# Performance work log

Hardware: AMD Instinct MI355X
Metric: run time of the kernel (lower is better)

Reference implementation:

```python
import jax, jax.numpy as jnp
import numpy as np

IMG = 224   # img_size
K = 8       # num_bands
E = 256     # embed_dim


def _radial_masks(size, k):
    # Faithful to torch _create_radial_masks: center = size//2, max_r = size/sqrt(2)
    center = size // 2
    y, x = jnp.meshgrid(jnp.arange(size), jnp.arange(size), indexing='ij')
    r = jnp.sqrt(((x - center) ** 2 + (y - center) ** 2).astype(jnp.float32))
    max_r = size / np.sqrt(2.0)
    step = np.float32(max_r / k)
    i = jnp.arange(k, dtype=jnp.float32)[:, None, None]
    masks = ((r[None] >= step * i) & (r[None] < step * (i + 1.0))).astype(jnp.float32)
    return masks  # [K, H, W]


def setup_inputs() -> dict:
    key = jax.random.key(0)
    ks = jax.random.split(key, 3)
    x = jax.random.normal(ks[0], (64, 3, IMG, IMG), dtype=jnp.float32)
    W1 = jax.random.normal(ks[1], (3, E), dtype=jnp.float32) * 0.3
    b1 = jnp.zeros((E,), jnp.float32)
    gamma = jnp.ones((E,), jnp.float32)
    beta = jnp.zeros((E,), jnp.float32)
    W2 = jax.random.normal(ks[2], (E, E), dtype=jnp.float32) * (1.0 / np.sqrt(E))
    b2 = jnp.zeros((E,), jnp.float32)
    return {"x": x, "W1": W1, "b1": b1, "gamma": gamma, "beta": beta, "W2": W2, "b2": b2}


def reference(x, W1, b1, gamma, beta, W2, b2):
    masks = _radial_masks(IMG, K)                    # [K,H,W], binary, non-overlapping
    x_gray = x.mean(axis=1)                          # [B,H,W]
    fft = jnp.fft.fftshift(jnp.fft.fft2(x_gray), axes=(-2, -1))
    mag = jnp.log1p(jnp.abs(fft))                    # log(1+|F|)
    mu = mag.mean(axis=(1, 2), keepdims=True)
    sd = jnp.std(mag, axis=(1, 2), keepdims=True, ddof=1) + 1e-6  # torch .std is unbiased
    magn = (mag - mu) / sd                           # [B,H,W]

    msum = masks.sum(axis=(1, 2))                    # [K], true mask pixel counts
    mask_sums = msum + 1e-6
    s1 = jnp.einsum('bhw,khw->bk', magn, masks)      # per-band sum
    s2 = jnp.einsum('bhw,khw->bk', magn * magn, masks)
    means = s1 / mask_sums
    # sum((magn - means)^2 * mask) = s2 - 2*means*s1 + means^2 * msum  (exact expansion)
    var_num = s2 - 2.0 * means * s1 + (means ** 2) * msum
    stds = jnp.sqrt(var_num / mask_sums + 1e-6)
    # masked_fill(mask==0, -1e9) then amax over H,W
    maxs = jnp.max(jnp.where(masks[None] > 0, magn[:, None], -1e9), axis=(2, 3))

    feats = jnp.stack([means, stds, maxs], axis=-1)  # [B,K,3]
    h = feats @ W1 + b1                              # [B,K,E]
    hm = h.mean(axis=-1, keepdims=True)
    hv = h.var(axis=-1, keepdims=True)
    h = (h - hm) / jnp.sqrt(hv + 1e-5) * gamma + beta  # LayerNorm, eps=1e-5
    h = jax.nn.relu(h)
    return h @ W2 + b2                               # [B,K,E]
```

## Files before the change

### kernel.cpp

```cpp
#include <hip/hip_runtime.h>
#include <math.h>

#define IMG 224
#define NPIX 50176
#define BATCH 64
#define EDIM 256

typedef _Float16 f16;
typedef __attribute__((ext_vector_type(8))) _Float16 f16x8;
typedef __attribute__((ext_vector_type(4))) _Float16 f16x4;
typedef __attribute__((ext_vector_type(4))) float f32x4;
typedef unsigned int u32;


#define GLD16(gp, lp)                                                          \
  __builtin_amdgcn_global_load_lds(                                            \
      (const __attribute__((address_space(1))) u32*)(gp),                      \
      (__attribute__((address_space(3))) u32*)(lp), 16, 0, 0)

__global__ __launch_bounds__(256) void gemmA_kernel(const float* __restrict__ x,
                                                    const f16* __restrict__ B1,
                                                    f16* __restrict__ B2t) {
  __shared__ f16 As[2][64][64];
  __shared__ f16 Bs[2][256][64];
  int m0 = blockIdx.x * 64;
  int tid = threadIdx.x;
  int lane = tid & 63, wid = tid >> 6;
  int wr = wid >> 1, wc = wid & 1;

  int arow = tid >> 2;
  int aseg = tid & 3;
  int am = m0 + arow;
  int ab = am / 224, ah = am - ab * 224;
  const float* px = x + (size_t)ab * 3 * NPIX + ah * IMG;
  int s0 = (aseg * 2) ^ (arow & 7);
  int s1 = (aseg * 2 + 1) ^ (arow & 7);

  int srow = lane >> 3;
  int sk8 = (lane & 7) ^ srow;

  f32x4 xl[3][4];

  f32x4 acc[2][8];
#pragma unroll
  for (int i = 0; i < 2; ++i)
#pragma unroll
    for (int j = 0; j < 8; ++j) acc[i][j] = (f32x4){0.f, 0.f, 0.f, 0.f};

  auto issueA = [&](int t) {
    int kb = t * 64 + aseg * 16;
    if (kb < 224) {
#pragma unroll
      for (int c = 0; c < 3; ++c)
#pragma unroll
        for (int q = 0; q < 4; ++q)
          xl[c][q] = *(const f32x4*)(px + c * NPIX + kb + q * 4);
    }
  };
  auto issueB = [&](int bufi, int t) {
    int k0 = t * 64;
#pragma unroll
    for (int ci = 0; ci < 8; ++ci) {
      int j = wid * 8 + ci;
      GLD16(B1 + (size_t)(j * 8 + srow) * 256 + k0 + sk8 * 8,
            &Bs[bufi][0][0] + j * 512);
    }
  };
  auto writeA = [&](int bufi, int t) {
    int kb = t * 64 + aseg * 16;
    f16x8 h0, h1;
    if (kb < 224) {
#pragma unroll
      for (int j = 0; j < 8; ++j) {
        int q = j >> 2, r = j & 3;
        h0[j] = (f16)((xl[0][q][r] + xl[1][q][r] + xl[2][q][r]) * (1.0f / 3.0f));
      }
#pragma unroll
      for (int j = 0; j < 8; ++j) {
        int q = 2 + (j >> 2), r = j & 3;
        h1[j] = (f16)((xl[0][q][r] + xl[1][q][r] + xl[2][q][r]) * (1.0f / 3.0f));
      }
    } else {
#pragma unroll
      for (int j = 0; j < 8; ++j) { h0[j] = (f16)0.f; h1[j] = (f16)0.f; }
    }
    *(f16x8*)&As[bufi][arow][s0 * 8] = h0;
    *(f16x8*)&As[bufi][arow][s1 * 8] = h1;
  };

  issueA(0);
  issueB(0, 0);
#pragma unroll 1
  for (int t = 0; t < 4; ++t) {
    int cur = t & 1;
    asm volatile("s_waitcnt vmcnt(0)" ::: "memory");
    writeA(cur, t);
    asm volatile("s_waitcnt lgkmcnt(0)" ::: "memory");
    __builtin_amdgcn_s_barrier();
    if (t < 3) { issueA(t + 1); issueB(cur ^ 1, t + 1); }
#pragma unroll
    for (int kk = 0; kk < 2; ++kk) {
      f16x8 af[2], bfr[8];
#pragma unroll
      for (int mi = 0; mi < 2; ++mi) {
        int row = wr * 32 + mi * 16 + (lane & 15);
        int slot = (kk * 4 + (lane >> 4)) ^ (row & 7);
        af[mi] = *(const f16x8*)&As[cur][row][slot * 8];
      }
#pragma unroll
      for (int nj = 0; nj < 8; ++nj) {
        int row = wc * 128 + nj * 16 + (lane & 15);
        int slot = (kk * 4 + (lane >> 4)) ^ (row & 7);
        bfr[nj] = *(const f16x8*)&Bs[cur][row][slot * 8];
      }
#pragma unroll
      for (int mi = 0; mi < 2; ++mi)
#pragma unroll
        for (int nj = 0; nj < 8; ++nj)
          acc[mi][nj] = __builtin_amdgcn_mfma_f32_16x16x32_f16(
              af[mi], bfr[nj], acc[mi][nj], 0, 0, 0);
    }
    __builtin_amdgcn_s_barrier();
  }

  int mbase = m0 + wr * 32, nbase = wc * 128;
#pragma unroll
  for (int mi = 0; mi < 2; ++mi) {
#pragma unroll
    for (int nj = 0; nj < 8; ++nj) {
      int c = nbase + nj * 16 + (lane & 15);
      if (c >= 226) continue;
      int m = mbase + mi * 16 + ((lane >> 4) << 2);
      int b = m / 224;
      int h = m - b * 224;
      int v = c, kb = h;
      if (c >= 113) { v = c - 113; kb = 224 + h; }
      size_t off = (size_t)(b * 128 + v) * 448 + kb;
      f32x4 y = acc[mi][nj];
      f16x4 hv;
#pragma unroll
      for (int r = 0; r < 4; ++r) hv[r] = (f16)y[r];
      *(f16x4*)&B2t[off] = hv;
    }
  }
}

template <int LDK, int NT>
__device__ __forceinline__ void gemm_core(const f16* __restrict__ A,
                                          const f16* __restrict__ B,
                                          int m0, int n0,
                                          f16 (*As)[64][64], f16 (*Bs)[128][64],
                                          f32x4 acc[2][4]) {
  int tid = threadIdx.x;
  int lane = tid & 63, wid = tid >> 6;
  int wr = wid >> 1, wc = wid & 1;
  int srow = lane >> 3;
  int sk8 = (lane & 7) ^ srow;

  auto stage = [&](int bufi, int t) {
    int k0 = t * 64;
#pragma unroll
    for (int ci = 0; ci < 6; ++ci) {
      int c = wid * 6 + ci;
      if (c < 8) {
        GLD16(A + (size_t)(m0 + c * 8 + srow) * LDK + k0 + sk8 * 8,
              &As[bufi][0][0] + c * 512);
      } else {
        int j = c - 8;
        GLD16(B + (size_t)(n0 + j * 8 + srow) * LDK + k0 + sk8 * 8,
              &Bs[bufi][0][0] + j * 512);
      }
    }
  };

  stage(0, 0);
#pragma unroll 1
  for (int t = 0; t < NT; ++t) {
    int cur = t & 1;
    if (t + 1 < NT) {
      stage(cur ^ 1, t + 1);
      asm volatile("s_waitcnt vmcnt(6)" ::: "memory");
    } else {
      asm volatile("s_waitcnt vmcnt(0)" ::: "memory");
    }
    __builtin_amdgcn_s_barrier();
#pragma unroll
    for (int kk = 0; kk < 2; ++kk) {
      f16x8 af[2], bfr[4];
#pragma unroll
      for (int mi = 0; mi < 2; ++mi) {
        int row = wr * 32 + mi * 16 + (lane & 15);
        int slot = (kk * 4 + (lane >> 4)) ^ (row & 7);
        af[mi] = *(const f16x8*)&As[cur][row][slot * 8];
      }
#pragma unroll
      for (int nj = 0; nj < 4; ++nj) {
        int row = wc * 64 + nj * 16 + (lane & 15);
        int slot = (kk * 4 + (lane >> 4)) ^ (row & 7);
        bfr[nj] = *(const f16x8*)&Bs[cur][row][slot * 8];
      }
#pragma unroll
      for (int mi = 0; mi < 2; ++mi)
#pragma unroll
        for (int nj = 0; nj < 4; ++nj)
          acc[mi][nj] = __builtin_amdgcn_mfma_f32_16x16x32_f16(
              af[mi], bfr[nj], acc[mi][nj], 0, 0, 0);
    }
    __builtin_amdgcn_s_barrier();
  }
}

__global__ __launch_bounds__(256) void gemmB_kernel(const f16* __restrict__ W2h,
                                                    const f16* __restrict__ B2t,
                                                    float* __restrict__ stats) {
  __shared__ f16 As[2][64][64];
  __shared__ f16 Bs[2][128][64];
  int b = blockIdx.x;
  int m0 = blockIdx.y * 64;
  f32x4 acc[2][4];
#pragma unroll
  for (int i = 0; i < 2; ++i)
#pragma unroll
    for (int j = 0; j < 4; ++j) acc[i][j] = (f32x4){0.f, 0.f, 0.f, 0.f};

  gemm_core<448, 7>(W2h, B2t + (size_t)b * 128 * 448, m0, 0, As, Bs, acc);

  int tid = threadIdx.x;
  int lane = tid & 63, wid = tid >> 6;
  int wr = wid >> 1, wc = wid & 1;
  int rbase = m0 + wr * 32;
  const float step = (float)(158.39191898578665 / 8.0);

  float gsum = 0.f, gsq = 0.f;
  float s1[8] = {0}, s2[8] = {0}, cnt[8] = {0};
  float mx[8] = {0, 0, 0, 0, 0, 0, 0, 0};

#pragma unroll
  for (int mi = 0; mi < 2; ++mi) {
#pragma unroll
    for (int nj = 0; nj < 4; ++nj) {
      int n = wc * 64 + nj * 16 + (lane & 15);
      if (n >= 113) continue;
      float wgt = (n >= 1 && n <= 111) ? 2.f : 1.f;
      float dx2 = (float)(n * n);
      int rr = rbase + mi * 16 + ((lane >> 4) << 2);
      f32x4 f = acc[mi][nj];
#pragma unroll
      for (int p = 0; p < 2; ++p) {
        int u = (rr >> 1) + p;
        float re = f[2 * p], im = f[2 * p + 1];
        float mv = log1pf(sqrtf(re * re + im * im));
        int a = (u <= 111) ? u : 224 - u;
        float r = sqrtf((float)(a * a) + dx2);
        int bd = 255;
#pragma unroll
        for (int k = 0; k < 8; k++) {
          float lo = step * (float)k;
          float hi = step * (float)(k + 1);
          if (r >= lo && r < hi) bd = k;
        }
        float wm = wgt * mv;
        gsum += wm;
        gsq += wm * mv;
#pragma unroll
        for (int k = 0; k < 8; k++) {
          bool m = (bd == k);
          s1[k] += m ? wm : 0.f;
          s2[k] += m ? wm * mv : 0.f;
          cnt[k] += m ? wgt : 0.f;
          mx[k] = m ? fmaxf(mx[k], mv) : mx[k];
        }
      }
    }
  }

  float vals[34];
  vals[0] = gsum; vals[1] = gsq;
#pragma unroll
  for (int k = 0; k < 8; k++) {
    vals[2 + k] = s1[k]; vals[10 + k] = s2[k]; vals[18 + k] = mx[k]; vals[26 + k] = cnt[k];
  }
#pragma unroll
  for (int i = 0; i < 34; i++) {
    float v = vals[i];
    const bool isMax = (i >= 18 && i < 26);
#pragma unroll
    for (int off = 32; off > 0; off >>= 1) {
      float o = __shfl_down(v, off);
      v = isMax ? fmaxf(v, o) : (v + o);
    }
    vals[i] = v;
  }
  float* red = (float*)&As[0][0][0];
  if ((tid & 63) == 0) {
#pragma unroll
    for (int i = 0; i < 34; i++) red[wid * 34 + i] = vals[i];
  }
  __syncthreads();
  if (tid < 34) {
    bool isMax = (tid >= 18 && tid < 26);
    float v = red[tid];
#pragma unroll
    for (int ww = 1; ww < 4; ww++) {
      float o = red[ww * 34 + tid];
      v = isMax ? fmaxf(v, o) : (v + o);
    }
    if (isMax)
      atomicMax((u32*)&stats[b * 34 + tid], __float_as_uint(v));
    else
      atomicAdd(&stats[b * 34 + tid], v);
  }
}

__global__ __launch_bounds__(256) void prep_kernel(f16* __restrict__ B1,
                                                   f16* __restrict__ W2h,
                                                   f16* __restrict__ B2t,
                                                   float* __restrict__ stats) {
  int blk = blockIdx.x;
  int tid = threadIdx.x;
  if (blk < 256) {
    int n = blk, k = tid;
    float val = 0.f;
    if (k < 224 && n < 226) {
      int v = (n < 113) ? n : n - 113;
      int m = (k * v) % 224;
      float mf = (float)m / 112.0f;
      val = (n < 113) ? cospif(mf) : -sinpif(mf);
    }
    B1[n * 256 + k] = (f16)val;
  } else if (blk < 1040) {
    int i = (blk - 256) * 256 + tid;
    int row = i / 448;
    int k = i - row * 448;
    int u = row >> 1;
    bool imrow = row & 1;
    bool kim = k >= 224;
    int kk = kim ? k - 224 : k;
    int m = (u * kk) % 224;
    float mf = (float)m / 112.0f;
    float c = cospif(mf), s = sinpif(mf);
    float val = imrow ? (kim ? c : -s) : (kim ? s : c);
    W2h[i] = (f16)val;
  } else if (blk < 1880) {
    int w = (blk - 1040) * 256 + tid;
    int img = w / 3360;
    int off = w - img * 3360;
    ((u32*)B2t)[(size_t)(img * 128 + 113) * 224 + off] = 0;
  } else {
    int i = (blk - 1880) * 256 + tid;
    if (i < BATCH * 34) stats[i] = 0.f;
  }
}

__global__ __launch_bounds__(256) void mlp_kernel(const float* __restrict__ stats,
                                                  const float* __restrict__ W1,
                                                  const float* __restrict__ b1,
                                                  const float* __restrict__ gamma,
                                                  const float* __restrict__ beta,
                                                  const float* __restrict__ W2m,
                                                  const float* __restrict__ b2,
                                                  float* __restrict__ out) {
  int bk = blockIdx.x;
  int b = bk >> 3, k = bk & 7;
  int e = threadIdx.x;

  __shared__ float st[34];
  if (e < 34) st[e] = stats[b * 34 + e];
  __syncthreads();

  const float N = (float)NPIX;
  float mu = st[0] / N;
  float varg = fmaxf(st[1] - N * mu * mu, 0.0f) / (N - 1.0f);
  float sd = sqrtf(varg) + 1e-6f;

  float s1r = st[2 + k], s2r = st[10 + k], mxr = st[18 + k], cntk = st[26 + k];
  float ms = cntk + 1e-6f;
  float s1n = (s1r - mu * cntk) / sd;
  float s2n = (s2r - 2.0f * mu * s1r + mu * mu * cntk) / (sd * sd);
  float mean_k = s1n / ms;
  float var_num = s2n - 2.0f * mean_k * s1n + mean_k * mean_k * cntk;
  float std_k = sqrtf(var_num / ms + 1e-6f);
  float max_k = (mxr - mu) / sd;

  float h = mean_k * W1[e] + std_k * W1[EDIM + e] + max_k * W1[2 * EDIM + e] + b1[e];

  float s = h, q = h * h;
#pragma unroll
  for (int off = 32; off > 0; off >>= 1) {
    s += __shfl_down(s, off);
    q += __shfl_down(q, off);
  }
  __shared__ float rs[4], rq[4];
  __shared__ float hmS, hvS;
  if ((e & 63) == 0) { rs[e >> 6] = s; rq[e >> 6] = q; }
  __syncthreads();
  if (e == 0) {
    float ts = rs[0] + rs[1] + rs[2] + rs[3];
    float tq = rq[0] + rq[1] + rq[2] + rq[3];
    float hm = ts / 256.0f;
    hmS = hm;
    hvS = fmaxf(tq / 256.0f - hm * hm, 0.0f);
  }
  __syncthreads();
  float hn = (h - hmS) / sqrtf(hvS + 1e-5f) * gamma[e] + beta[e];
  float hr = fmaxf(hn, 0.0f);

  __shared__ float hs[EDIM];
  hs[e] = hr;
  __syncthreads();

  float acc = b2[e];
#pragma unroll 8
  for (int j = 0; j < EDIM; j++) acc += hs[j] * W2m[j * EDIM + e];
  out[(size_t)bk * EDIM + e] = acc;
}

extern "C" void kernel_launch(void* const* d_in, const int* in_sizes, int n_in,
                              void* d_out, int out_size, void* d_ws, size_t ws_size,
                              hipStream_t stream) {
  const float* x     = (const float*)d_in[0];
  const float* W1    = (const float*)d_in[1];
  const float* b1    = (const float*)d_in[2];
  const float* gamma = (const float*)d_in[3];
  const float* beta  = (const float*)d_in[4];
  const float* W2m   = (const float*)d_in[5];
  const float* b2    = (const float*)d_in[6];
  float* out = (float*)d_out;

  char* W = (char*)d_ws;
  f16* B2t = (f16*)W;
  f16* B1  = (f16*)(W + 7340032);
  f16* W2h = (f16*)(W + 7340032 + 131072);
  float* stats = (float*)(W + 7340032 + 131072 + 401408);

  prep_kernel<<<dim3(1889), dim3(256), 0, stream>>>(B1, W2h, B2t, stats);
  gemmA_kernel<<<dim3(224), dim3(256), 0, stream>>>(x, B1, B2t);
  gemmB_kernel<<<dim3(BATCH, 7), dim3(256), 0, stream>>>(W2h, B2t, stats);
  mlp_kernel<<<dim3(BATCH * 8), dim3(256), 0, stream>>>(stats, W1, b1, gamma, beta, W2m, b2, out);
}
```

Baseline: 56.54 us.

## Generate DFT twiddles in-kernel from LDS cosine table, drop prep kernel

The separate prep kernel, which wrote the DFT twiddle matrices and padding to global memory, is removed. Both GEMM kernels now build their twiddle tiles directly in shared memory from a 224-entry cosine table, walking the index modulo 224. gemmB also moves to a triple-buffered B pipeline with a remapped 1D block order, and stats zeroing moves into gemmA block 0. This saves one kernel launch and the global writes and reads of the twiddle matrices. In exchange it adds per-tile integer and LDS-gather work, and it no longer zeroes the B2t padding rows, which only feed output columns that are discarded.

```diff
diff --git a/kernel.cpp b/kernel.cpp
--- a/kernel.cpp
+++ b/kernel.cpp
@@ -19,14 +19,23 @@
       (__attribute__((address_space(3))) u32*)(lp), 16, 0, 0)
 
 __global__ __launch_bounds__(256) void gemmA_kernel(const float* __restrict__ x,
-                                                    const f16* __restrict__ B1,
-                                                    f16* __restrict__ B2t) {
+                                                    f16* __restrict__ B2t,
+                                                    float* __restrict__ stats) {
+  __shared__ float T[224];
   __shared__ f16 As[2][64][64];
   __shared__ f16 Bs[2][256][64];
   int m0 = blockIdx.x * 64;
   int tid = threadIdx.x;
   int lane = tid & 63, wid = tid >> 6;
   int wr = wid >> 1, wc = wid & 1;
+
+  if (blockIdx.x == 0) {
+#pragma unroll
+    for (int i = 0; i < 9; ++i) {
+      int idx = i * 256 + tid;
+      if (idx < BATCH * 34) stats[idx] = 0.f;
+    }
+  }
 
   int arow = tid >> 2;
   int aseg = tid & 3;
@@ -36,11 +45,7 @@
   int s0 = (aseg * 2) ^ (arow & 7);
   int s1 = (aseg * 2 + 1) ^ (arow & 7);
 
-  int srow = lane >> 3;
-  int sk8 = (lane & 7) ^ srow;
-
   f32x4 xl[3][4];
-
   f32x4 acc[2][8];
 #pragma unroll
   for (int i = 0; i < 2; ++i)
@@ -55,15 +60,6 @@
 #pragma unroll
         for (int q = 0; q < 4; ++q)
           xl[c][q] = *(const f32x4*)(px + c * NPIX + kb + q * 4);
-    }
-  };
-  auto issueB = [&](int bufi, int t) {
-    int k0 = t * 64;
-#pragma unroll
-    for (int ci = 0; ci < 8; ++ci) {
-      int j = wid * 8 + ci;
-      GLD16(B1 + (size_t)(j * 8 + srow) * 256 + k0 + sk8 * 8,
-            &Bs[bufi][0][0] + j * 512);
     }
   };
   auto writeA = [&](int bufi, int t) {
@@ -87,9 +83,28 @@
     *(f16x8*)&As[bufi][arow][s0 * 8] = h0;
     *(f16x8*)&As[bufi][arow][s1 * 8] = h1;
   };
+  auto computeB = [&](int bufi, int t) {
+    int row = tid;
+    int v = (row < 113) ? row : row - 113;
+    u32 off = (row < 113) ? 0u : 56u;
+    u32 idx = ((u32)(t * 64) * (u32)v + off) % 224u;
+#pragma unroll
+    for (int g = 0; g < 8; ++g) {
+      f16x8 hv;
+#pragma unroll
+      for (int j = 0; j < 8; ++j) {
+        hv[j] = (f16)T[idx];
+        idx += v; if (idx >= 224u) idx -= 224u;
+      }
+      *(f16x8*)&Bs[bufi][row][(g ^ (row & 7)) * 8] = hv;
+    }
+  };
 
   issueA(0);
-  issueB(0, 0);
+  if (tid < 224) T[tid] = cospif((float)tid / 112.0f);
+  __syncthreads();
+  computeB(0, 0);
+
 #pragma unroll 1
   for (int t = 0; t < 4; ++t) {
     int cur = t & 1;
@@ -97,7 +112,7 @@
     writeA(cur, t);
     asm volatile("s_waitcnt lgkmcnt(0)" ::: "memory");
     __builtin_amdgcn_s_barrier();
-    if (t < 3) { issueA(t + 1); issueB(cur ^ 1, t + 1); }
+    if (t < 3) { issueA(t + 1); computeB(cur ^ 1, t + 1); }
 #pragma unroll
     for (int kk = 0; kk < 2; ++kk) {
       f16x8 af[2], bfr[8];
@@ -145,45 +160,82 @@
   }
 }
 
-template <int LDK, int NT>
-__device__ __forceinline__ void gemm_core(const f16* __restrict__ A,
-                                          const f16* __restrict__ B,
-                                          int m0, int n0,
-                                          f16 (*As)[64][64], f16 (*Bs)[128][64],
-                                          f32x4 acc[2][4]) {
+__global__ __launch_bounds__(256) void gemmB_kernel(const f16* __restrict__ B2t,
+                                                    float* __restrict__ stats) {
+  __shared__ float T[224];
+  __shared__ f16 As[2][64][64];
+  __shared__ f16 Bs[3][128][64];
   int tid = threadIdx.x;
   int lane = tid & 63, wid = tid >> 6;
   int wr = wid >> 1, wc = wid & 1;
+
+  int bid = blockIdx.x;
+  int nb = (bid & 7) * 56 + (bid >> 3);
+  int b = nb / 7;
+  int m0 = (nb - b * 7) * 64;
+  const f16* Bb = B2t + (size_t)b * 128 * 448;
+
   int srow = lane >> 3;
   int sk8 = (lane & 7) ^ srow;
 
-  auto stage = [&](int bufi, int t) {
+  f32x4 acc[2][4];
+#pragma unroll
+  for (int i = 0; i < 2; ++i)
+#pragma unroll
+    for (int j = 0; j < 4; ++j) acc[i][j] = (f32x4){0.f, 0.f, 0.f, 0.f};
+
+  auto issueB = [&](int t) {
     int k0 = t * 64;
-#pragma unroll
-    for (int ci = 0; ci < 6; ++ci) {
-      int c = wid * 6 + ci;
-      if (c < 8) {
-        GLD16(A + (size_t)(m0 + c * 8 + srow) * LDK + k0 + sk8 * 8,
-              &As[bufi][0][0] + c * 512);
-      } else {
-        int j = c - 8;
-        GLD16(B + (size_t)(n0 + j * 8 + srow) * LDK + k0 + sk8 * 8,
-              &Bs[bufi][0][0] + j * 512);
-      }
+    int bi = t % 3;
+#pragma unroll
+    for (int ci = 0; ci < 4; ++ci) {
+      int j = wid * 4 + ci;
+      GLD16(Bb + (size_t)(j * 8 + srow) * 448 + k0 + sk8 * 8,
+            &Bs[bi][0][0] + j * 512);
     }
   };
-
-  stage(0, 0);
+  auto computeA = [&](int bufi, int t) {
+    int row = tid >> 2, seg = tid & 3;
+    int rr = m0 + row;
+    u32 u = (u32)(rr >> 1);
+    int imrow = rr & 1;
+    int kb = t * 64 + seg * 16;
+    int kim = kb >= 224;
+    u32 kq = (u32)(kb - (kim ? 224 : 0));
+    u32 off = imrow ? (kim ? 0u : 56u) : (kim ? 168u : 0u);
+    u32 idx = (u * kq + off) % 224u;
+#pragma unroll
+    for (int g = 0; g < 2; ++g) {
+      f16x8 hv;
+#pragma unroll
+      for (int j = 0; j < 8; ++j) {
+        hv[j] = (f16)T[idx];
+        idx += u; if (idx >= 224u) idx -= 224u;
+      }
+      int lg = seg * 2 + g;
+      *(f16x8*)&As[bufi][row][(lg ^ (row & 7)) * 8] = hv;
+    }
+  };
+
+  if (tid < 224) T[tid] = cospif((float)tid / 112.0f);
+  issueB(0);
+  issueB(1);
+  __syncthreads();
+  computeA(0, 0);
+
 #pragma unroll 1
-  for (int t = 0; t < NT; ++t) {
+  for (int t = 0; t < 7; ++t) {
     int cur = t & 1;
-    if (t + 1 < NT) {
-      stage(cur ^ 1, t + 1);
-      asm volatile("s_waitcnt vmcnt(6)" ::: "memory");
+    if (t < 6) {
+      asm volatile("s_waitcnt vmcnt(4)" ::: "memory");
     } else {
       asm volatile("s_waitcnt vmcnt(0)" ::: "memory");
     }
+    asm volatile("s_waitcnt lgkmcnt(0)" ::: "memory");
     __builtin_amdgcn_s_barrier();
+    if (t + 2 <= 6) issueB(t + 2);
+    if (t < 6) computeA(cur ^ 1, t + 1);
+    int bcur = t % 3;
 #pragma unroll
     for (int kk = 0; kk < 2; ++kk) {
       f16x8 af[2], bfr[4];
@@ -197,7 +249,7 @@
       for (int nj = 0; nj < 4; ++nj) {
         int row = wc * 64 + nj * 16 + (lane & 15);
         int slot = (kk * 4 + (lane >> 4)) ^ (row & 7);
-        bfr[nj] = *(const f16x8*)&Bs[cur][row][slot * 8];
+        bfr[nj] = *(const f16x8*)&Bs[bcur][row][slot * 8];
       }
 #pragma unroll
       for (int mi = 0; mi < 2; ++mi)
@@ -208,29 +260,9 @@
     }
     __builtin_amdgcn_s_barrier();
   }
-}
-
-__global__ __launch_bounds__(256) void gemmB_kernel(const f16* __restrict__ W2h,
-                                                    const f16* __restrict__ B2t,
-                                                    float* __restrict__ stats) {
-  __shared__ f16 As[2][64][64];
-  __shared__ f16 Bs[2][128][64];
-  int b = blockIdx.x;
-  int m0 = blockIdx.y * 64;
-  f32x4 acc[2][4];
-#pragma unroll
-  for (int i = 0; i < 2; ++i)
-#pragma unroll
-    for (int j = 0; j < 4; ++j) acc[i][j] = (f32x4){0.f, 0.f, 0.f, 0.f};
-
-  gemm_core<448, 7>(W2h, B2t + (size_t)b * 128 * 448, m0, 0, As, Bs, acc);
-
-  int tid = threadIdx.x;
-  int lane = tid & 63, wid = tid >> 6;
-  int wr = wid >> 1, wc = wid & 1;
+
   int rbase = m0 + wr * 32;
   const float step = (float)(158.39191898578665 / 8.0);
-
   float gsum = 0.f, gsq = 0.f;
   float s1[8] = {0}, s2[8] = {0}, cnt[8] = {0};
   float mx[8] = {0, 0, 0, 0, 0, 0, 0, 0};
@@ -309,46 +341,6 @@
       atomicMax((u32*)&stats[b * 34 + tid], __float_as_uint(v));
     else
       atomicAdd(&stats[b * 34 + tid], v);
-  }
-}
-
-__global__ __launch_bounds__(256) void prep_kernel(f16* __restrict__ B1,
-                                                   f16* __restrict__ W2h,
-                                                   f16* __restrict__ B2t,
-                                                   float* __restrict__ stats) {
-  int blk = blockIdx.x;
-  int tid = threadIdx.x;
-  if (blk < 256) {
-    int n = blk, k = tid;
-    float val = 0.f;
-    if (k < 224 && n < 226) {
-      int v = (n < 113) ? n : n - 113;
-      int m = (k * v) % 224;
-      float mf = (float)m / 112.0f;
-      val = (n < 113) ? cospif(mf) : -sinpif(mf);
-    }
-    B1[n * 256 + k] = (f16)val;
-  } else if (blk < 1040) {
-    int i = (blk - 256) * 256 + tid;
-    int row = i / 448;
-    int k = i - row * 448;
-    int u = row >> 1;
-    bool imrow = row & 1;
-    bool kim = k >= 224;
-    int kk = kim ? k - 224 : k;
-    int m = (u * kk) % 224;
-    float mf = (float)m / 112.0f;
-    float c = cospif(mf), s = sinpif(mf);
-    float val = imrow ? (kim ? c : -s) : (kim ? s : c);
-    W2h[i] = (f16)val;
-  } else if (blk < 1880) {
-    int w = (blk - 1040) * 256 + tid;
-    int img = w / 3360;
-    int off = w - img * 3360;
-    ((u32*)B2t)[(size_t)(img * 128 + 113) * 224 + off] = 0;
-  } else {
-    int i = (blk - 1880) * 256 + tid;
-    if (i < BATCH * 34) stats[i] = 0.f;
   }
 }
 
@@ -429,12 +421,9 @@
 
   char* W = (char*)d_ws;
   f16* B2t = (f16*)W;
-  f16* B1  = (f16*)(W + 7340032);
-  f16* W2h = (f16*)(W + 7340032 + 131072);
-  float* stats = (float*)(W + 7340032 + 131072 + 401408);
-
-  prep_kernel<<<dim3(1889), dim3(256), 0, stream>>>(B1, W2h, B2t, stats);
-  gemmA_kernel<<<dim3(224), dim3(256), 0, stream>>>(x, B1, B2t);
-  gemmB_kernel<<<dim3(BATCH, 7), dim3(256), 0, stream>>>(W2h, B2t, stats);
+  float* stats = (float*)(W + 7340032);
+
+  gemmA_kernel<<<dim3(224), dim3(256), 0, stream>>>(x, B2t, stats);
+  gemmB_kernel<<<dim3(448), dim3(256), 0, stream>>>(B2t, stats);
   mlp_kernel<<<dim3(BATCH * 8), dim3(256), 0, stream>>>(stats, W1, b1, gamma, beta, W2m, b2, out);
 }
```

Measured after the change: 54.84 us. 1.03x faster.
